# Kernel optimization log

Hardware: AMD Instinct MI355X
Metric: run time of the kernel (lower is better)

## Reference

```python
import jax, jax.numpy as jnp
import numpy as np

MD = 4  # max displacement / pad size
NEG_SLOPE = 0.1

def setup_inputs() -> dict:
    key = jax.random.key(0)
    k0, k1 = jax.random.split(key)
    B, C, H, W = 8, 256, 96, 128
    in0 = jax.random.normal(k0, (B, C, H, W), dtype=jnp.float32)
    in1 = jax.random.normal(k1, (B, C, H, W), dtype=jnp.float32)
    return {"in0": in0, "in1": in1}

def _correlation(x1, x2, md=MD):
    # PWC-Net style cost volume: for each displacement d in [-md, md]^2,
    # out[:, d, h, w] = mean_c x1[:, c, h, w] * x2[:, c, h+dy, w+dx]
    # (kernel_size=1, stride1=stride2=1, normalized by channel count)
    B, C, H, W = x1.shape
    x2p = jnp.pad(x2, ((0, 0), (0, 0), (md, md), (md, md)))
    slices = []
    for dy in range(2 * md + 1):          # fixed 9x9 displacement grid
        for dx in range(2 * md + 1):
            shifted = jax.lax.dynamic_slice(x2p, (0, 0, dy, dx), (B, C, H, W))
            slices.append(jnp.mean(x1 * shifted, axis=1))  # [B, H, W]
    return jnp.stack(slices, axis=1)      # [B, 81, H, W]

def reference(in0, in1):
    corr = _correlation(in0, in1, MD)
    return jax.nn.leaky_relu(corr, NEG_SLOPE)
```

## Files before the change

### kernel.cpp

```cpp
#include <hip/hip_runtime.h>


#define B_ 8
#define C_ 256
#define H_ 96
#define W_ 128
#define TH 2
#define CC 8
#define NCH (C_ / CC)
#define HW (H_ * W_)
#define CHSTRIDE (CC * HW)
#define S2SZ (TH * 544)
#define S1SZ (TH * 512)
#define SMSZ (S2SZ + S1SZ)
#define NTHR 64

typedef __fp16 h2_t __attribute__((ext_vector_type(2)));
union H2U { unsigned int u; h2_t h; };

__device__ __forceinline__ h2_t u_as_h2(unsigned int u) { H2U x; x.u = u; return x.h; }

__device__ __forceinline__ unsigned int packh2(float a, float b) {
    H2U x; x.h = __builtin_amdgcn_cvt_pkrtz(a, b); return x.u;
}

#if __has_builtin(__builtin_amdgcn_fdot2)
__device__ __forceinline__ float dot2(unsigned int a, unsigned int b, float c) {
    return __builtin_amdgcn_fdot2(u_as_h2(a), u_as_h2(b), c, false);
}
#else
__device__ __forceinline__ float dot2(unsigned int a, unsigned int b, float c) {
    h2_t ha = u_as_h2(a), hb = u_as_h2(b);
    return c + (float)ha[0] * (float)hb[0] + (float)ha[1] * (float)hb[1];
}
#endif

__global__ __attribute__((amdgpu_flat_work_group_size(NTHR, NTHR)))
void corr_kernel(const float* __restrict__ x1, const float* __restrict__ x2,
                 float* __restrict__ out)
{
    __shared__ __align__(16) unsigned int smem[SMSZ];

    const int b   = blockIdx.x;
    const int dy  = blockIdx.y;
    const int h0  = blockIdx.z * TH;
    const int lane = threadIdx.x;
    const int hr  = lane >> 5;
    const int wq  = lane & 31;

    const int rx = hr, w4 = wq;
    const unsigned off1 =
        (unsigned)(b * C_) * HW + (unsigned)((h0 + rx) * W_ + 4 * w4);
    const int c1 = S2SZ + rx * 512 + (w4 >> 1) * 32;
    const int X1 = (4 * (w4 & 1)) ^ ((w4 >> 1) & 7) ^ rx;

    const int r2 = hr, g = wq + 1;
    const int h2 = h0 + dy + r2 - 4;
    const bool val2 = (h2 >= 0) && (h2 < H_);
    const unsigned off2 =
        (unsigned)(b * C_) * HW + (unsigned)((val2 ? h2 : 0) * W_ + 4 * g - 4);
    const int c2 = r2 * 544 + (g >> 1) * 32;
    const int X2 = (4 * (g & 1)) ^ ((g >> 1) & 7) ^ r2;

    const int base1 = S2SZ + hr * 512 + (wq >> 1) * 32;
    const int S1X   = (4 * (wq & 1)) ^ ((wq >> 1) & 7) ^ hr;

    int a2p[6];
    #pragma unroll
    for (int t = 0; t < 12; t += 2) {
        const int s0 = 4 * wq + t, s1 = s0 + 1;
        const int A0 = hr * 544 + (s0 >> 3) * 32
                     + (((s0 & 7) ^ ((s0 >> 3) & 7) ^ hr) << 2);
        const int A1 = hr * 544 + (s1 >> 3) * 32
                     + (((s1 & 7) ^ ((s1 >> 3) & 7) ^ hr) << 2);
        a2p[t >> 1] = A0 | (A1 << 16);
    }

    float acc[4][9];
    #pragma unroll
    for (int p = 0; p < 4; ++p)
        #pragma unroll
        for (int d = 0; d < 9; ++d) acc[p][d] = 0.f;

    #pragma unroll
    for (int i = 0; i < S2SZ / NTHR; ++i) smem[lane + i * NTHR] = 0u;
    __syncthreads();

    #pragma unroll 1
    for (int cc = 0; cc < NCH; ++cc) {
        const unsigned co = (unsigned)cc * (unsigned)CHSTRIDE;
        {
            const float* p = x1 + off1 + co;
            const float4 f0 = *reinterpret_cast<const float4*>(p);
            const float4 f1 = *reinterpret_cast<const float4*>(p + HW);
            const float4 f2 = *reinterpret_cast<const float4*>(p + 2 * HW);
            const float4 f3 = *reinterpret_cast<const float4*>(p + 3 * HW);
            const float4 f4 = *reinterpret_cast<const float4*>(p + 4 * HW);
            const float4 f5 = *reinterpret_cast<const float4*>(p + 5 * HW);
            const float4 f6 = *reinterpret_cast<const float4*>(p + 6 * HW);
            const float4 f7 = *reinterpret_cast<const float4*>(p + 7 * HW);
            uint4 wv;
            wv.x = packh2(f0.x, f1.x); wv.y = packh2(f2.x, f3.x);
            wv.z = packh2(f4.x, f5.x); wv.w = packh2(f6.x, f7.x);
            *reinterpret_cast<uint4*>(&smem[c1 + ((0 ^ X1) << 2)]) = wv;
            wv.x = packh2(f0.y, f1.y); wv.y = packh2(f2.y, f3.y);
            wv.z = packh2(f4.y, f5.y); wv.w = packh2(f6.y, f7.y);
            *reinterpret_cast<uint4*>(&smem[c1 + ((1 ^ X1) << 2)]) = wv;
            wv.x = packh2(f0.z, f1.z); wv.y = packh2(f2.z, f3.z);
            wv.z = packh2(f4.z, f5.z); wv.w = packh2(f6.z, f7.z);
            *reinterpret_cast<uint4*>(&smem[c1 + ((2 ^ X1) << 2)]) = wv;
            wv.x = packh2(f0.w, f1.w); wv.y = packh2(f2.w, f3.w);
            wv.z = packh2(f4.w, f5.w); wv.w = packh2(f6.w, f7.w);
            *reinterpret_cast<uint4*>(&smem[c1 + ((3 ^ X1) << 2)]) = wv;
        }
        if (val2) {
            const float* p = x2 + off2 + co;
            const float4 f0 = *reinterpret_cast<const float4*>(p);
            const float4 f1 = *reinterpret_cast<const float4*>(p + HW);
            const float4 f2 = *reinterpret_cast<const float4*>(p + 2 * HW);
            const float4 f3 = *reinterpret_cast<const float4*>(p + 3 * HW);
            const float4 f4 = *reinterpret_cast<const float4*>(p + 4 * HW);
            const float4 f5 = *reinterpret_cast<const float4*>(p + 5 * HW);
            const float4 f6 = *reinterpret_cast<const float4*>(p + 6 * HW);
            const float4 f7 = *reinterpret_cast<const float4*>(p + 7 * HW);
            uint4 wv;
            wv.x = packh2(f0.x, f1.x); wv.y = packh2(f2.x, f3.x);
            wv.z = packh2(f4.x, f5.x); wv.w = packh2(f6.x, f7.x);
            *reinterpret_cast<uint4*>(&smem[c2 + ((0 ^ X2) << 2)]) = wv;
            wv.x = packh2(f0.y, f1.y); wv.y = packh2(f2.y, f3.y);
            wv.z = packh2(f4.y, f5.y); wv.w = packh2(f6.y, f7.y);
            *reinterpret_cast<uint4*>(&smem[c2 + ((1 ^ X2) << 2)]) = wv;
            wv.x = packh2(f0.z, f1.z); wv.y = packh2(f2.z, f3.z);
            wv.z = packh2(f4.z, f5.z); wv.w = packh2(f6.z, f7.z);
            *reinterpret_cast<uint4*>(&smem[c2 + ((2 ^ X2) << 2)]) = wv;
            wv.x = packh2(f0.w, f1.w); wv.y = packh2(f2.w, f3.w);
            wv.z = packh2(f4.w, f5.w); wv.w = packh2(f6.w, f7.w);
            *reinterpret_cast<uint4*>(&smem[c2 + ((3 ^ X2) << 2)]) = wv;
        }
        __syncthreads();

        uint4 x1v[4];
        #pragma unroll
        for (int p = 0; p < 4; ++p)
            x1v[p] = *reinterpret_cast<const uint4*>(&smem[base1 + ((p ^ S1X) << 2)]);
        #pragma unroll
        for (int t = 0; t < 12; ++t) {
            const int ad = (t & 1) ? (a2p[t >> 1] >> 16) : (a2p[t >> 1] & 0xffff);
            const uint4 x2v = *reinterpret_cast<const uint4*>(&smem[ad]);
            #pragma unroll
            for (int p = 0; p < 4; ++p) {
                const int dxx = t - p;
                if (dxx >= 0 && dxx <= 8) {
                    float a = acc[p][dxx];
                    a = dot2(x1v[p].x, x2v.x, a);
                    a = dot2(x1v[p].y, x2v.y, a);
                    a = dot2(x1v[p].z, x2v.z, a);
                    a = dot2(x1v[p].w, x2v.w, a);
                    acc[p][dxx] = a;
                }
            }
        }
        __syncthreads();
    }

    const float inv = 1.0f / 256.0f;
    float* ob = out + (((size_t)(b * 81 + dy * 9)) * H_ + (h0 + hr)) * W_ + wq * 4;
    #pragma unroll
    for (int dxx = 0; dxx < 9; ++dxx) {
        float4 o;
        float v;
        v = acc[0][dxx] * inv; o.x = v >= 0.f ? v : 0.1f * v;
        v = acc[1][dxx] * inv; o.y = v >= 0.f ? v : 0.1f * v;
        v = acc[2][dxx] * inv; o.z = v >= 0.f ? v : 0.1f * v;
        v = acc[3][dxx] * inv; o.w = v >= 0.f ? v : 0.1f * v;
        *reinterpret_cast<float4*>(ob + (size_t)dxx * HW) = o;
    }
}

extern "C" void kernel_launch(void* const* d_in, const int* in_sizes, int n_in,
                              void* d_out, int out_size, void* d_ws, size_t ws_size,
                              hipStream_t stream) {
    const float* x1 = (const float*)d_in[0];
    const float* x2 = (const float*)d_in[1];
    float* out = (float*)d_out;
    corr_kernel<<<dim3(B_, 9, H_ / TH), dim3(NTHR), 0, stream>>>(x1, x2, out);
}
```

Baseline: 97.50 us.

## Share x2 tile across three dy rows per block; keep x1 in registers

Each block now handles three dy displacements using three wavefronts (192 threads). They share one staged x2 tile of four padded rows in LDS, which cuts redundant x2 global loads and conversions across dy. x1 is loaded straight into registers by every wave instead of going through shared memory, so x1 is read from global three times per block but LDS traffic and footprint shrink. The grid drops from 9 to 3 blocks along the dy axis, lowering block count and raising per-block work.

```diff
diff --git a/kernel.cpp b/kernel.cpp
--- a/kernel.cpp
+++ b/kernel.cpp
@@ -10,10 +10,8 @@
 #define NCH (C_ / CC)
 #define HW (H_ * W_)
 #define CHSTRIDE (CC * HW)
-#define S2SZ (TH * 544)
-#define S1SZ (TH * 512)
-#define SMSZ (S2SZ + S1SZ)
-#define NTHR 64
+#define S2SZ (4 * 544)
+#define NTHR 192
 
 typedef __fp16 h2_t __attribute__((ext_vector_type(2)));
 union H2U { unsigned int u; h2_t h; };
@@ -39,40 +37,39 @@
 void corr_kernel(const float* __restrict__ x1, const float* __restrict__ x2,
                  float* __restrict__ out)
 {
-    __shared__ __align__(16) unsigned int smem[SMSZ];
+    __shared__ __align__(16) unsigned int smem[S2SZ];
 
     const int b   = blockIdx.x;
-    const int dy  = blockIdx.y;
-    const int h0  = blockIdx.z * TH;
-    const int lane = threadIdx.x;
+    const int h0  = blockIdx.y * TH;
+    const int dg  = blockIdx.z;
+    const int tid = threadIdx.x;
+    const int wid = tid >> 6;
+    const int lane = tid & 63;
     const int hr  = lane >> 5;
     const int wq  = lane & 31;
 
-    const int rx = hr, w4 = wq;
-    const unsigned off1 =
-        (unsigned)(b * C_) * HW + (unsigned)((h0 + rx) * W_ + 4 * w4);
-    const int c1 = S2SZ + rx * 512 + (w4 >> 1) * 32;
-    const int X1 = (4 * (w4 & 1)) ^ ((w4 >> 1) & 7) ^ rx;
+    const unsigned o1 =
+        (unsigned)(b * C_) * HW + (unsigned)((h0 + hr) * W_ + 4 * wq);
 
-    const int r2 = hr, g = wq + 1;
-    const int h2 = h0 + dy + r2 - 4;
-    const bool val2 = (h2 >= 0) && (h2 < H_);
-    const unsigned off2 =
-        (unsigned)(b * C_) * HW + (unsigned)((val2 ? h2 : 0) * W_ + 4 * g - 4);
+    const bool x2act = (tid < 128);
+    const int r2 = (tid >> 5) & 3;
+    const int g  = (tid & 31) + 1;
+    const int h2 = h0 + 3 * dg + r2 - 4;
+    const bool val2 = x2act && (h2 >= 0) && (h2 < H_);
+    const unsigned off2 = (unsigned)(b * C_) * HW
+        + (unsigned)((val2 ? h2 : 0) * W_ + 4 * g - 4);
     const int c2 = r2 * 544 + (g >> 1) * 32;
-    const int X2 = (4 * (g & 1)) ^ ((g >> 1) & 7) ^ r2;
+    const int X2 = (4 * (g & 1)) ^ ((g >> 1) & 7) ^ (r2 & 7);
 
-    const int base1 = S2SZ + hr * 512 + (wq >> 1) * 32;
-    const int S1X   = (4 * (wq & 1)) ^ ((wq >> 1) & 7) ^ hr;
-
+    const int row = hr + wid;
     int a2p[6];
     #pragma unroll
     for (int t = 0; t < 12; t += 2) {
         const int s0 = 4 * wq + t, s1 = s0 + 1;
-        const int A0 = hr * 544 + (s0 >> 3) * 32
-                     + (((s0 & 7) ^ ((s0 >> 3) & 7) ^ hr) << 2);
-        const int A1 = hr * 544 + (s1 >> 3) * 32
-                     + (((s1 & 7) ^ ((s1 >> 3) & 7) ^ hr) << 2);
+        const int A0 = row * 544 + (s0 >> 3) * 32
+                     + (((s0 & 7) ^ ((s0 >> 3) & 7) ^ row) << 2);
+        const int A1 = row * 544 + (s1 >> 3) * 32
+                     + (((s1 & 7) ^ ((s1 >> 3) & 7) ^ row) << 2);
         a2p[t >> 1] = A0 | (A1 << 16);
     }
 
@@ -82,37 +79,37 @@
         #pragma unroll
         for (int d = 0; d < 9; ++d) acc[p][d] = 0.f;
 
-    #pragma unroll
-    for (int i = 0; i < S2SZ / NTHR; ++i) smem[lane + i * NTHR] = 0u;
+    for (int i = tid; i < S2SZ; i += NTHR) smem[i] = 0u;
     __syncthreads();
 
     #pragma unroll 1
     for (int cc = 0; cc < NCH; ++cc) {
         const unsigned co = (unsigned)cc * (unsigned)CHSTRIDE;
+
+        uint4 x1v[4];
         {
-            const float* p = x1 + off1 + co;
-            const float4 f0 = *reinterpret_cast<const float4*>(p);
-            const float4 f1 = *reinterpret_cast<const float4*>(p + HW);
-            const float4 f2 = *reinterpret_cast<const float4*>(p + 2 * HW);
-            const float4 f3 = *reinterpret_cast<const float4*>(p + 3 * HW);
-            const float4 f4 = *reinterpret_cast<const float4*>(p + 4 * HW);
-            const float4 f5 = *reinterpret_cast<const float4*>(p + 5 * HW);
-            const float4 f6 = *reinterpret_cast<const float4*>(p + 6 * HW);
-            const float4 f7 = *reinterpret_cast<const float4*>(p + 7 * HW);
-            uint4 wv;
-            wv.x = packh2(f0.x, f1.x); wv.y = packh2(f2.x, f3.x);
-            wv.z = packh2(f4.x, f5.x); wv.w = packh2(f6.x, f7.x);
-            *reinterpret_cast<uint4*>(&smem[c1 + ((0 ^ X1) << 2)]) = wv;
-            wv.x = packh2(f0.y, f1.y); wv.y = packh2(f2.y, f3.y);
-            wv.z = packh2(f4.y, f5.y); wv.w = packh2(f6.y, f7.y);
-            *reinterpret_cast<uint4*>(&smem[c1 + ((1 ^ X1) << 2)]) = wv;
-            wv.x = packh2(f0.z, f1.z); wv.y = packh2(f2.z, f3.z);
-            wv.z = packh2(f4.z, f5.z); wv.w = packh2(f6.z, f7.z);
-            *reinterpret_cast<uint4*>(&smem[c1 + ((2 ^ X1) << 2)]) = wv;
-            wv.x = packh2(f0.w, f1.w); wv.y = packh2(f2.w, f3.w);
-            wv.z = packh2(f4.w, f5.w); wv.w = packh2(f6.w, f7.w);
-            *reinterpret_cast<uint4*>(&smem[c1 + ((3 ^ X1) << 2)]) = wv;
+            const float* p1 = x1 + o1 + co;
+            const float4 f0 = *reinterpret_cast<const float4*>(p1);
+            const float4 f1 = *reinterpret_cast<const float4*>(p1 + HW);
+            const float4 f2 = *reinterpret_cast<const float4*>(p1 + 2 * HW);
+            const float4 f3 = *reinterpret_cast<const float4*>(p1 + 3 * HW);
+            x1v[0].x = packh2(f0.x, f1.x); x1v[1].x = packh2(f0.y, f1.y);
+            x1v[2].x = packh2(f0.z, f1.z); x1v[3].x = packh2(f0.w, f1.w);
+            x1v[0].y = packh2(f2.x, f3.x); x1v[1].y = packh2(f2.y, f3.y);
+            x1v[2].y = packh2(f2.z, f3.z); x1v[3].y = packh2(f2.w, f3.w);
         }
+        {
+            const float* p1 = x1 + o1 + co + 4 * HW;
+            const float4 f4 = *reinterpret_cast<const float4*>(p1);
+            const float4 f5 = *reinterpret_cast<const float4*>(p1 + HW);
+            const float4 f6 = *reinterpret_cast<const float4*>(p1 + 2 * HW);
+            const float4 f7 = *reinterpret_cast<const float4*>(p1 + 3 * HW);
+            x1v[0].z = packh2(f4.x, f5.x); x1v[1].z = packh2(f4.y, f5.y);
+            x1v[2].z = packh2(f4.z, f5.z); x1v[3].z = packh2(f4.w, f5.w);
+            x1v[0].w = packh2(f6.x, f7.x); x1v[1].w = packh2(f6.y, f7.y);
+            x1v[2].w = packh2(f6.z, f7.z); x1v[3].w = packh2(f6.w, f7.w);
+        }
+
         if (val2) {
             const float* p = x2 + off2 + co;
             const float4 f0 = *reinterpret_cast<const float4*>(p);
@@ -139,10 +136,6 @@
         }
         __syncthreads();
 
-        uint4 x1v[4];
-        #pragma unroll
-        for (int p = 0; p < 4; ++p)
-            x1v[p] = *reinterpret_cast<const uint4*>(&smem[base1 + ((p ^ S1X) << 2)]);
         #pragma unroll
         for (int t = 0; t < 12; ++t) {
             const int ad = (t & 1) ? (a2p[t >> 1] >> 16) : (a2p[t >> 1] & 0xffff);
@@ -164,6 +157,7 @@
     }
 
     const float inv = 1.0f / 256.0f;
+    const int dy = 3 * dg + wid;
     float* ob = out + (((size_t)(b * 81 + dy * 9)) * H_ + (h0 + hr)) * W_ + wq * 4;
     #pragma unroll
     for (int dxx = 0; dxx < 9; ++dxx) {
@@ -183,5 +177,5 @@
     const float* x1 = (const float*)d_in[0];
     const float* x2 = (const float*)d_in[1];
     float* out = (float*)d_out;
-    corr_kernel<<<dim3(B_, 9, H_ / TH), dim3(NTHR), 0, stream>>>(x1, x2, out);
+    corr_kernel<<<dim3(B_, H_ / TH, 3), dim3(NTHR), 0, stream>>>(x1, x2, out);
 }
```

Result: slower. 119.5 us (+22.5%).
